# Kernel tuning notes

Hardware: AMD Instinct MI355X
Metric: run time of the kernel (lower is better)

The kernel has to match this reference:

```python
import jax, jax.numpy as jnp
import numpy as np

B, L, D, M = 8, 4096, 512, 64


def setup_inputs() -> dict:
    key = jax.random.key(0)
    k1, k2, k3 = jax.random.split(key, 3)
    scale = 1.0 / (D * D)
    return {
        "q": jax.random.normal(k1, (B, L, D), dtype=jnp.float32),
        "w_real": scale * jax.random.normal(k2, (D, D, M), dtype=jnp.float32),
        "w_imag": scale * jax.random.normal(k3, (D, D, M), dtype=jnp.float32),
    }


def reference(q, w_real, w_imag):
    # q: [B, L, D]; weights: [D, D, modes]
    b, l, d = q.shape
    n_freq = l // 2 + 1
    q_ft = jnp.fft.rfft(q, axis=1)                      # [B, n_freq, D] complex64
    m = min(w_real.shape[-1], n_freq)
    W = w_real[..., :m] + 1j * w_imag[..., :m]          # [D, E, m] complex
    # Batched over modes: replaces the per-mode python loop with one einsum.
    out_m = jnp.einsum('bmd,dem->bme', q_ft[:, :m, :], W)  # [B, m, D]
    out_ft = jnp.zeros((b, n_freq, d), dtype=q_ft.dtype).at[:, :m, :].set(out_m)
    return jnp.fft.irfft(out_ft, n=l, axis=1)           # [B, L, D] float32
```

## Files before the change

### kernel.cpp

```cpp
#include <hip/hip_runtime.h>

#define B_ 8
#define L_ 4096
#define D_ 512
#define M_ 64

typedef __attribute__((ext_vector_type(8))) short bh8;
typedef __attribute__((ext_vector_type(4))) float f4;
typedef __attribute__((ext_vector_type(4))) unsigned u32x4;

__device__ inline unsigned short f2bf(float f) {
  unsigned u = __float_as_uint(f);
  return (unsigned short)((u + 0x7fffu + ((u >> 16) & 1u)) >> 16);
}
__device__ inline unsigned packbf(float lo, float hi) {
  return (unsigned)f2bf(lo) | ((unsigned)f2bf(hi) << 16);
}

__global__ void k_ftab(unsigned short* __restrict__ F) {
  int t = blockIdx.x * 256 + threadIdx.x;
  int r = t >> 12, l = t & 4095;
  int k = r & 63, part = r >> 6;
  int ph = (k * l) & (L_ - 1);
  double ang = 6.283185307179586476925286766559 * (double)ph / (double)L_;
  float v = part ? (float)(-sin(ang)) : (float)(cos(ang));
  F[t] = f2bf(v);
}

__global__ void k_gtab(unsigned short* __restrict__ G) {
  int t = blockIdx.x * 256 + threadIdx.x;
  int l = t >> 7, j = t & 127;
  int k = j & 63, part = j >> 6;
  int ph = (k * l) & (L_ - 1);
  double ang = 6.283185307179586476925286766559 * (double)ph / (double)L_;
  double ck = (k == 0 ? 1.0 : 2.0) / (double)L_;
  float v = part ? (float)(-ck * sin(ang)) : (float)(ck * cos(ang));
  G[t] = f2bf(v);
}

__global__ __launch_bounds__(512, 4) void k_dft_mfma(
    const float* __restrict__ q, const unsigned short* __restrict__ F,
    float* __restrict__ pQ) {
  int tid = threadIdx.x;
  int dt = blockIdx.x, b = blockIdx.y, kc = blockIdx.z;
  int d0 = dt * 64;
  int lbase = kc * 512;

  int w = tid >> 6, lane = tid & 63;
  int mh = w & 3, nc = w >> 2;
  int lr = lane & 15, kg = lane >> 4;

  f4 acc[2][2];
#pragma unroll
  for (int i = 0; i < 2; ++i)
#pragma unroll
    for (int j = 0; j < 2; ++j) { f4 z = {0.f, 0.f, 0.f, 0.f}; acc[i][j] = z; }

  const unsigned short* A0 = F + (size_t)(mh * 32 + lr) * 4096 + lbase + kg * 8;
  const unsigned short* A1 = A0 + (size_t)16 * 4096;
  const float* q0 = q + ((size_t)b * L_ + lbase + kg * 8) * D_ + d0 + nc * 32 + lr;

#pragma unroll 2
  for (int s = 0; s < 16; ++s) {
    const float* qs = q0 + (size_t)s * 32 * D_;
    float v0[8], v1[8];
#pragma unroll
    for (int j = 0; j < 8; ++j) {
      v0[j] = qs[(size_t)j * D_];
      v1[j] = qs[(size_t)j * D_ + 16];
    }
    union { u32x4 u; bh8 h; } bf0, bf1;
    bf0.u.x = packbf(v0[0], v0[1]); bf0.u.y = packbf(v0[2], v0[3]);
    bf0.u.z = packbf(v0[4], v0[5]); bf0.u.w = packbf(v0[6], v0[7]);
    bf1.u.x = packbf(v1[0], v1[1]); bf1.u.y = packbf(v1[2], v1[3]);
    bf1.u.z = packbf(v1[4], v1[5]); bf1.u.w = packbf(v1[6], v1[7]);
    bh8 af0 = *(const bh8*)(A0 + s * 32);
    bh8 af1 = *(const bh8*)(A1 + s * 32);
    acc[0][0] = __builtin_amdgcn_mfma_f32_16x16x32_bf16(af0, bf0.h, acc[0][0], 0, 0, 0);
    acc[0][1] = __builtin_amdgcn_mfma_f32_16x16x32_bf16(af0, bf1.h, acc[0][1], 0, 0, 0);
    acc[1][0] = __builtin_amdgcn_mfma_f32_16x16x32_bf16(af1, bf0.h, acc[1][0], 0, 0, 0);
    acc[1][1] = __builtin_amdgcn_mfma_f32_16x16x32_bf16(af1, bf1.h, acc[1][1], 0, 0, 0);
  }

#pragma unroll
  for (int mi = 0; mi < 2; ++mi) {
    int r = mh * 32 + mi * 16 + kg * 4;
#pragma unroll
    for (int ni = 0; ni < 2; ++ni) {
      int d = d0 + nc * 32 + ni * 16 + lr;
#pragma unroll
      for (int j = 0; j < 4; ++j)
        pQ[(((size_t)kc * 128 + (r + j)) * 8 + b) * 512 + d] = acc[mi][ni][j];
    }
  }
}

__global__ __launch_bounds__(256) void k_red2(const float* __restrict__ pQ,
                                              unsigned* __restrict__ Qbf) {
  int g = blockIdx.x * 256 + threadIdx.x;
  int dq = g & 127;
  int b = (g >> 7) & 7;
  int k = g >> 10;
  f4 sr = {0.f, 0.f, 0.f, 0.f}, si = {0.f, 0.f, 0.f, 0.f};
#pragma unroll
  for (int kc = 0; kc < 8; ++kc) {
    size_t base = (((size_t)kc * 128 + k) * 8 + b) * 512 + dq * 4;
    sr += *(const f4*)(pQ + base);
    si += *(const f4*)(pQ + base + (size_t)64 * 8 * 512);
  }
  u32x4 o;
  o.x = packbf(sr[0], si[0]); o.y = packbf(sr[1], si[1]);
  o.z = packbf(sr[2], si[2]); o.w = packbf(sr[3], si[3]);
  *(u32x4*)(Qbf + ((size_t)k * 8 + b) * 512 + dq * 4) = o;
}

__global__ __launch_bounds__(256, 2) void k_mix_mfma(
    const float* __restrict__ wr_, const float* __restrict__ wi_,
    const unsigned* __restrict__ Qbf, float* __restrict__ pOut) {
  __shared__ unsigned Wlds[4 * 4096];

  int tid = threadIdx.x;
  int et = blockIdx.x, dc = blockIdx.y, kh = blockIdx.z;
  int e0 = et * 16;
  int w = tid >> 6, lane = tid & 63;
  int er = lane & 15, kg = lane >> 4;
  int part = er >> 3, b = er & 7;
  int dh = w & 1;
  int ksl = kh * 32 + (w >> 1) * 16;
  unsigned* wbuf = Wlds + w * 4096;

  int dL = lane >> 4;
  int eL = (lane >> 2) & 3;
  int kq = lane & 3;

  f4 acc[16];
#pragma unroll
  for (int t = 0; t < 16; ++t) { f4 z = {0.f, 0.f, 0.f, 0.f}; acc[t] = z; }

  const unsigned* qbase = Qbf + ((size_t)ksl * 8 + b) * 512 + kg * 4;

#define DSFENCE() do {                                        \
    asm volatile("s_waitcnt lgkmcnt(0)" ::: "memory");        \
    __builtin_amdgcn_sched_barrier(0);                        \
  } while (0)

#pragma unroll 1
  for (int r = 0; r < 2; ++r) {
    int dbase = dc * 64 + r * 32 + dh * 16;

    u32x4 qv[16];
#pragma unroll
    for (int kl = 0; kl < 16; ++kl)
      qv[kl] = *(const u32x4*)(qbase + (size_t)kl * 4096 + dbase);
    __builtin_amdgcn_sched_barrier(0);

#pragma unroll 1
    for (int s = 0; s < 2; ++s) {
      float4 vr[8], vi[8];
#pragma unroll
      for (int i = 0; i < 8; ++i) {
        int d = dbase + s * 8 + dL + (i & 1) * 4;
        int e = e0 + eL + (i >> 1) * 4;
        size_t gb = ((size_t)d * 512 + e) * 64 + ksl + kq * 4;
        vr[i] = *(const float4*)(wr_ + gb);
        vi[i] = *(const float4*)(wi_ + gb);
      }
#pragma unroll
      for (int i = 0; i < 8; ++i) {
        int ee = eL + (i >> 1) * 4;
        int dd = s * 8 + dL + (i & 1) * 4;
        int ddp = dd ^ (kq << 2);
        unsigned* o = wbuf + ee * 16 + ddp;
        o[(kq * 4 + 0) * 256] = packbf(vr[i].x, vi[i].x);
        o[(kq * 4 + 1) * 256] = packbf(vr[i].y, vi[i].y);
        o[(kq * 4 + 2) * 256] = packbf(vr[i].z, vi[i].z);
        o[(kq * 4 + 3) * 256] = packbf(vr[i].w, vi[i].w);
      }
    }
    DSFENCE();

#pragma unroll
    for (int kl = 0; kl < 16; ++kl) {
      union { u32x4 u; bh8 h; } av, bv;
      av.u = *(const u32x4*)(wbuf + kl * 256 + er * 16 + ((kg ^ (kl >> 2)) << 2));
      u32x4 q = qv[kl];
      if (part == 0) {
        bv.u.x = q.x ^ 0x80000000u; bv.u.y = q.y ^ 0x80000000u;
        bv.u.z = q.z ^ 0x80000000u; bv.u.w = q.w ^ 0x80000000u;
      } else {
        bv.u.x = (q.x >> 16) | (q.x << 16); bv.u.y = (q.y >> 16) | (q.y << 16);
        bv.u.z = (q.z >> 16) | (q.z << 16); bv.u.w = (q.w >> 16) | (q.w << 16);
      }
      acc[kl] = __builtin_amdgcn_mfma_f32_16x16x32_bf16(av.h, bv.h, acc[kl], 0, 0, 0);
    }
    DSFENCE();
  }
#undef DSFENCE

#pragma unroll
  for (int kl = 0; kl < 16; ++kl) {
    int kglob = ksl + kl;
    size_t off = (size_t)(dc * 2 + dh) * 524288 +
                 (((size_t)kglob * 2 + part) * 8 + b) * 512 + e0 + kg * 4;
    *(f4*)(pOut + off) = acc[kl];
  }
}

__global__ __launch_bounds__(512) void k_psum2(const float* __restrict__ pOut,
                                               unsigned* __restrict__ Pw) {
  __shared__ float sP[128 * 33];
  int tid = threadIdx.x;
  int e0 = blockIdx.x * 32, b = blockIdx.y;
  {
    int e = tid & 31, g = tid >> 5;
#pragma unroll
    for (int ii = 0; ii < 8; ++ii) {
      int col = g * 8 + ii;
      int rkp = ((col & 63) << 1) | (col >> 6);
      float s = 0.f;
#pragma unroll
      for (int c = 0; c < 16; ++c)
        s += pOut[(size_t)c * 524288 + (size_t)rkp * 4096 + b * 512 + e0 + e];
      sP[col * 33 + e] = s;
    }
  }
  __syncthreads();
  {
    int e = tid >> 4, c = tid & 15;
    size_t wbase = (((size_t)b * 512 + e0 + e) * 128 + c * 8) >> 1;
#pragma unroll
    for (int ii = 0; ii < 4; ++ii) {
      int col = c * 8 + ii * 2;
      Pw[wbase + ii] = packbf(sP[col * 33 + e], sP[(col + 1) * 33 + e]);
    }
  }
}

#define LST 72
__global__ __launch_bounds__(256, 2) void k_inv_mfma(
    const short* __restrict__ G, const short* __restrict__ P,
    float* __restrict__ y) {
  __shared__ short lds[2 * 128 * LST];
  short* As = lds;
  short* Bs = lds + 128 * LST;

  int tid = threadIdx.x;
  int lt = blockIdx.x, et = blockIdx.y, b = blockIdx.z;
  int l0 = lt * 128, e0 = et * 128;

  int wv = tid >> 6, lane = tid & 63;
  int wrow = wv >> 1, wcol = wv & 1;
  int lr = lane & 15, kg = lane >> 4;

  const short* Gb = G + (size_t)l0 * 128;
  const short* Pb = P + (size_t)b * D_ * 128 + (size_t)e0 * 128;

  f4 acc[4][4];
#pragma unroll
  for (int mi = 0; mi < 4; ++mi)
#pragma unroll
    for (int ni = 0; ni < 4; ++ni) {
      f4 z = {0.f, 0.f, 0.f, 0.f};
      acc[mi][ni] = z;
    }

#pragma unroll
  for (int kh = 0; kh < 2; ++kh) {
    if (kh) __syncthreads();
#pragma unroll
    for (int i = 0; i < 4; ++i) {
      int idx = i * 256 + tid;
      int row = idx >> 3, c = idx & 7;
      *(uint4*)(As + row * LST + c * 8) =
          *(const uint4*)(Gb + (size_t)row * 128 + kh * 64 + c * 8);
      *(uint4*)(Bs + row * LST + c * 8) =
          *(const uint4*)(Pb + (size_t)row * 128 + kh * 64 + c * 8);
    }
    __syncthreads();

#pragma unroll
    for (int ks = 0; ks < 2; ++ks) {
      bh8 a[4], bf[4];
#pragma unroll
      for (int i = 0; i < 4; ++i) {
        a[i]  = *(const bh8*)(As + (wrow * 64 + i * 16 + lr) * LST + ks * 32 + kg * 8);
        bf[i] = *(const bh8*)(Bs + (wcol * 64 + i * 16 + lr) * LST + ks * 32 + kg * 8);
      }
#pragma unroll
      for (int mi = 0; mi < 4; ++mi)
#pragma unroll
        for (int ni = 0; ni < 4; ++ni)
          acc[mi][ni] = __builtin_amdgcn_mfma_f32_16x16x32_bf16(
              a[mi], bf[ni], acc[mi][ni], 0, 0, 0);
    }
  }

#pragma unroll
  for (int mi = 0; mi < 4; ++mi) {
    int lg = l0 + wrow * 64 + mi * 16 + kg * 4;
#pragma unroll
    for (int ni = 0; ni < 4; ++ni) {
      int e = e0 + wcol * 64 + ni * 16 + lr;
#pragma unroll
      for (int j = 0; j < 4; ++j)
        y[((size_t)b * L_ + (lg + j)) * D_ + e] = acc[mi][ni][j];
    }
  }
}

extern "C" void kernel_launch(void* const* d_in, const int* in_sizes, int n_in,
                              void* d_out, int out_size, void* d_ws, size_t ws_size,
                              hipStream_t stream) {
  const float* q  = (const float*)d_in[0];
  const float* wr = (const float*)d_in[1];
  const float* wi = (const float*)d_in[2];
  float* out = (float*)d_out;
  char* ws = (char*)d_ws;

  unsigned short* Fbf = (unsigned short*)ws;
  unsigned short* Gbf = (unsigned short*)(ws + (1u << 20));
  unsigned* Qbf       = (unsigned*)(ws + (2u << 20));
  unsigned* Pw        = (unsigned*)(ws + (3u << 20));

  float* pQ   = out;
  float* pOut = out;

  hipLaunchKernelGGL(k_ftab, dim3((128 * L_) / 256), dim3(256), 0, stream, Fbf);
  hipLaunchKernelGGL(k_gtab, dim3((L_ * 128) / 256), dim3(256), 0, stream, Gbf);
  hipLaunchKernelGGL(k_dft_mfma, dim3(8, 8, 8), dim3(512), 0, stream,
                     q, Fbf, pQ);
  hipLaunchKernelGGL(k_red2, dim3(65536 / 256), dim3(256), 0, stream, pQ, Qbf);
  hipLaunchKernelGGL(k_mix_mfma, dim3(32, 8, 2), dim3(256), 0, stream,
                     wr, wi, Qbf, pOut);
  hipLaunchKernelGGL(k_psum2, dim3(16, 8), dim3(512), 0, stream, pOut, Pw);
  hipLaunchKernelGGL(k_inv_mfma, dim3(L_ / 128, D_ / 128, B_), dim3(256), 0,
                     stream, (const short*)Gbf, (const short*)Pw, out);
}
```

Baseline: 112.2 us.

## Repartition mode-mixing kernel into smaller per-wave tiles for higher occupancy

The mode-mixing MFMA kernel is restructured so each wave handles 8 frequency modes over a 16-wide d slice, instead of 16 modes over two d sub-slices. This halves the per-wave accumulator and LDS footprint, allows 4 blocks per CU, and doubles the grid along the d dimension. The partial-sum slab count stays at 16, so the downstream reduction is unchanged. The LDS XOR swizzle is dropped, which may add bank conflicts on the staged-weight reads, and each weight tile is now reused by fewer MFMAs.

```diff
diff --git a/kernel.cpp b/kernel.cpp
--- a/kernel.cpp
+++ b/kernel.cpp
@@ -114,10 +114,10 @@
   *(u32x4*)(Qbf + ((size_t)k * 8 + b) * 512 + dq * 4) = o;
 }
 
-__global__ __launch_bounds__(256, 2) void k_mix_mfma(
+__global__ __launch_bounds__(256, 4) void k_mix_mfma(
     const float* __restrict__ wr_, const float* __restrict__ wi_,
     const unsigned* __restrict__ Qbf, float* __restrict__ pOut) {
-  __shared__ unsigned Wlds[4 * 4096];
+  __shared__ unsigned Wlds[4 * 2048];
 
   int tid = threadIdx.x;
   int et = blockIdx.x, dc = blockIdx.y, kh = blockIdx.z;
@@ -125,17 +125,16 @@
   int w = tid >> 6, lane = tid & 63;
   int er = lane & 15, kg = lane >> 4;
   int part = er >> 3, b = er & 7;
-  int dh = w & 1;
-  int ksl = kh * 32 + (w >> 1) * 16;
-  unsigned* wbuf = Wlds + w * 4096;
-
-  int dL = lane >> 4;
-  int eL = (lane >> 2) & 3;
-  int kq = lane & 3;
-
-  f4 acc[16];
-#pragma unroll
-  for (int t = 0; t < 16; ++t) { f4 z = {0.f, 0.f, 0.f, 0.f}; acc[t] = z; }
+  int ksl = kh * 32 + w * 8;
+  unsigned* wbuf = Wlds + w * 2048;
+
+  int dd = lane >> 2;
+  int ee_lo = (lane >> 1) & 1;
+  int kq2 = lane & 1;
+
+  f4 acc[8];
+#pragma unroll
+  for (int t = 0; t < 8; ++t) { f4 z = {0.f, 0.f, 0.f, 0.f}; acc[t] = z; }
 
   const unsigned* qbase = Qbf + ((size_t)ksl * 8 + b) * 512 + kg * 4;
 
@@ -146,43 +145,39 @@
 
 #pragma unroll 1
   for (int r = 0; r < 2; ++r) {
-    int dbase = dc * 64 + r * 32 + dh * 16;
-
-    u32x4 qv[16];
-#pragma unroll
-    for (int kl = 0; kl < 16; ++kl)
+    int dbase = dc * 32 + r * 16;
+
+    u32x4 qv[8];
+#pragma unroll
+    for (int kl = 0; kl < 8; ++kl)
       qv[kl] = *(const u32x4*)(qbase + (size_t)kl * 4096 + dbase);
     __builtin_amdgcn_sched_barrier(0);
 
-#pragma unroll 1
-    for (int s = 0; s < 2; ++s) {
+    {
       float4 vr[8], vi[8];
 #pragma unroll
       for (int i = 0; i < 8; ++i) {
-        int d = dbase + s * 8 + dL + (i & 1) * 4;
-        int e = e0 + eL + (i >> 1) * 4;
-        size_t gb = ((size_t)d * 512 + e) * 64 + ksl + kq * 4;
+        int e = e0 + ee_lo + 2 * i;
+        size_t gb = ((size_t)(dbase + dd) * 512 + e) * 64 + ksl + kq2 * 4;
         vr[i] = *(const float4*)(wr_ + gb);
         vi[i] = *(const float4*)(wi_ + gb);
       }
 #pragma unroll
       for (int i = 0; i < 8; ++i) {
-        int ee = eL + (i >> 1) * 4;
-        int dd = s * 8 + dL + (i & 1) * 4;
-        int ddp = dd ^ (kq << 2);
-        unsigned* o = wbuf + ee * 16 + ddp;
-        o[(kq * 4 + 0) * 256] = packbf(vr[i].x, vi[i].x);
-        o[(kq * 4 + 1) * 256] = packbf(vr[i].y, vi[i].y);
-        o[(kq * 4 + 2) * 256] = packbf(vr[i].z, vi[i].z);
-        o[(kq * 4 + 3) * 256] = packbf(vr[i].w, vi[i].w);
+        int e_local = ee_lo + 2 * i;
+        unsigned* o = wbuf + (kq2 * 4) * 256 + e_local * 16 + dd;
+        o[0]   = packbf(vr[i].x, vi[i].x);
+        o[256] = packbf(vr[i].y, vi[i].y);
+        o[512] = packbf(vr[i].z, vi[i].z);
+        o[768] = packbf(vr[i].w, vi[i].w);
       }
     }
     DSFENCE();
 
 #pragma unroll
-    for (int kl = 0; kl < 16; ++kl) {
+    for (int kl = 0; kl < 8; ++kl) {
       union { u32x4 u; bh8 h; } av, bv;
-      av.u = *(const u32x4*)(wbuf + kl * 256 + er * 16 + ((kg ^ (kl >> 2)) << 2));
+      av.u = *(const u32x4*)(wbuf + kl * 256 + er * 16 + kg * 4);
       u32x4 q = qv[kl];
       if (part == 0) {
         bv.u.x = q.x ^ 0x80000000u; bv.u.y = q.y ^ 0x80000000u;
@@ -198,9 +193,9 @@
 #undef DSFENCE
 
 #pragma unroll
-  for (int kl = 0; kl < 16; ++kl) {
+  for (int kl = 0; kl < 8; ++kl) {
     int kglob = ksl + kl;
-    size_t off = (size_t)(dc * 2 + dh) * 524288 +
+    size_t off = (size_t)dc * 524288 +
                  (((size_t)kglob * 2 + part) * 8 + b) * 512 + e0 + kg * 4;
     *(f4*)(pOut + off) = acc[kl];
   }
@@ -330,7 +325,7 @@
   hipLaunchKernelGGL(k_dft_mfma, dim3(8, 8, 8), dim3(512), 0, stream,
                      q, Fbf, pQ);
   hipLaunchKernelGGL(k_red2, dim3(65536 / 256), dim3(256), 0, stream, pQ, Qbf);
-  hipLaunchKernelGGL(k_mix_mfma, dim3(32, 8, 2), dim3(256), 0, stream,
+  hipLaunchKernelGGL(k_mix_mfma, dim3(32, 16, 2), dim3(256), 0, stream,
                      wr, wi, Qbf, pOut);
   hipLaunchKernelGGL(k_psum2, dim3(16, 8), dim3(512), 0, stream, pOut, Pw);
   hipLaunchKernelGGL(k_inv_mfma, dim3(L_ / 128, D_ / 128, B_), dim3(256), 0,
```

Result: slower. 139.8 us (+24.6%).
